# Kernel optimization log

Measured on AMD Instinct MI355X. Metric: run time of the kernel, lower is better.

## Reference

```python
import jax, jax.numpy as jnp
import numpy as np
from jax import lax

B, S, D = 8, 96, 768
R, RSEQ, TAG = 24, 8, 3


def setup_inputs() -> dict:
    key = jax.random.key(0)
    k0, k1, k2, k3 = jax.random.split(key, 4)
    encoded_text = jax.random.normal(k0, (B, S, D), jnp.float32)
    rel_types_encoded = jax.random.normal(k1, (R, RSEQ, D), jnp.float32)
    proj_W = jax.random.normal(k2, (2 * D, 3 * D), jnp.float32) * 0.02
    proj_b = jnp.zeros((3 * D,), jnp.float32)
    rel_W = jax.random.normal(k3, (3 * D, R * TAG), jnp.float32) * 0.02
    rel_b = jnp.zeros((R * TAG,), jnp.float32)
    return {
        "encoded_text": encoded_text,
        "rel_types_encoded": rel_types_encoded,
        "proj_W": proj_W,
        "proj_b": proj_b,
        "rel_W": rel_W,
        "rel_b": rel_b,
    }


def _refine(enc, rel_types):
    """Faithful vectorized version of the nested python loops in
    get_encoded_text: for each sample i, R sequential cross-attention
    updates on matrix_b using matrix_a = rel_types_encoded[i] (the
    original code indexes with i, reusing the same matrix_a each step).
    enc: [Bsz, S, D]; rel_types: [R, RSEQ, D].
    """
    Bsz = enc.shape[0]
    d = enc.shape[-1]
    scale = 1.0 / jnp.sqrt(jnp.asarray(d, enc.dtype))
    num_steps = rel_types.shape[0]  # loop runs rel_types_encoded.size(0) times
    A_batch = rel_types[:Bsz]  # matrix_a = rel_types_encoded[i]

    def per_sample(b0, A):  # b0: [S, D], A: [RSEQ, D]
        def step(b, _):
            scores = (A @ b.T) * scale            # [RSEQ, S]
            w = jax.nn.softmax(scores, axis=-1)    # softmax over seq
            return b + w.T @ A, None               # matrix_b += matrix_c
        bf, _ = lax.scan(step, b0, None, length=num_steps)
        return bf

    return jax.vmap(per_sample)(enc, A_batch)


def reference(encoded_text, rel_types_encoded, proj_W, proj_b, rel_W, rel_b):
    enc = _refine(encoded_text, rel_types_encoded)  # [B, S, D]
    Bsz, seq, d = enc.shape
    rel_num = rel_types_encoded.shape[0]
    tag_size = rel_W.shape[1] // rel_num

    # projection(cat(head, tail)) == head @ Wh + tail @ Wt + b; avoid
    # materializing the [B, S*S, 2D] concat (same math as the original).
    Wh, Wt = proj_W[:d], proj_W[d:]
    Hh = enc @ Wh                                   # [B, S, 3D] head part
    Ht = enc @ Wt                                   # [B, S, 3D] tail part
    pairs = Hh[:, :, None, :] + Ht[:, None, :, :] + proj_b  # [B, S, S, 3D]
    pairs = jax.nn.relu(pairs)
    triple = pairs.reshape(Bsz, seq * seq, 3 * d) @ rel_W + rel_b
    triple = triple.reshape(Bsz, seq, seq, rel_num, tag_size)
    return jnp.transpose(triple, (0, 4, 3, 1, 2))  # [B, tag, rel, S, S]
```

## Files before the change

kernel.cpp:

```cpp
#include <hip/hip_runtime.h>
#include <hip/hip_bf16.h>
#include <math.h>
#include <stdint.h>
#include <string.h>

#define BB 8
#define SS 96
#define DD 768
#define RR 24
#define RSEQ 8
#define TAG 3
#define D3 2304
#define NC 72

typedef __attribute__((ext_vector_type(8))) short bf16x8;
typedef __attribute__((ext_vector_type(4))) float f32x4;
typedef _Float16 f16x8 __attribute__((ext_vector_type(8)));
typedef _Float16 f16x2 __attribute__((ext_vector_type(2)));

typedef __attribute__((address_space(3))) uint8_t lds_u8;
typedef const __attribute__((address_space(1))) uint8_t glb_u8;
static __device__ __forceinline__ void glld16(const void* g, void* l) {
  __builtin_amdgcn_global_load_lds((glb_u8*)g, (lds_u8*)l, 16, 0, 0);
}

#define VMW(N) asm volatile("s_waitcnt vmcnt(" #N ")" ::: "memory")

static __device__ inline uint32_t pkrhu(float lo, float hi) {
  uint32_t a, b;
  memcpy(&a, &lo, 4);
  memcpy(&b, &hi, 4);
  return __builtin_amdgcn_perm(b + 0x8000u, a + 0x8000u, 0x07060302u);
}
static __device__ inline uint32_t pkrne(float lo, float hi) {
  uint32_t a, b;
  memcpy(&a, &lo, 4);
  memcpy(&b, &hi, 4);
  a += 0x7FFFu + ((a >> 16) & 1u);
  b += 0x7FFFu + ((b >> 16) & 1u);
  return (a >> 16) | (b & 0xFFFF0000u);
}
static __device__ inline uint32_t pkf16(float lo, float hi) {
  union { f16x2 h; uint32_t u; } r;
  r.h[0] = (_Float16)lo;
  r.h[1] = (_Float16)hi;
  return r.u;
}
static __device__ inline uint16_t f16b(float v) {
  union { _Float16 h; uint16_t u; } r;
  r.h = (_Float16)v;
  return r.u;
}

__global__ __launch_bounds__(256) void k_prep0(const float* __restrict__ relW,
                                               uint16_t* __restrict__ Wb,
                                               const float* __restrict__ projW,
                                               uint16_t* __restrict__ Tp,
                                               const float* __restrict__ enc,
                                               const float* __restrict__ rel,
                                               float* __restrict__ SG) {
  __shared__ __align__(16) char smem[24704];
  const int blk = blockIdx.x;
  const int t = threadIdx.x;

  if (blk < 36) {
    float* tile = (float*)smem;
    const int k0 = blk * 64;
    const float* src = relW + (size_t)k0 * NC;
    for (int e = t; e < 64 * NC / 4; e += 256) ((float4*)tile)[e] = ((const float4*)src)[e];
    __syncthreads();
    for (int u = t; u < 80 * 16; u += 256) {
      const int n = u >> 4, kq = (u & 15) * 4;
      uint2 w = {0u, 0u};
      if (n < NC) {
        w.x = pkf16(tile[(kq + 0) * NC + n], tile[(kq + 1) * NC + n]);
        w.y = pkf16(tile[(kq + 2) * NC + n], tile[(kq + 3) * NC + n]);
      }
      *(uint2*)&Wb[(size_t)n * D3 + k0 + kq] = w;
    }
  } else if (blk < 900) {
    const int bx = blk - 36;
    float (*tile)[65] = (float(*)[65])smem;
    const int c0 = (bx % 36) * 64;
    const int r0 = (bx / 36) * 64;
    {
      const int tr = t >> 4;
      const int tc4 = (t & 15) * 4;
#pragma unroll
      for (int p = 0; p < 4; ++p) {
        const int r = tr + p * 16;
        const float4 v = *(const float4*)&projW[(size_t)(r0 + r) * D3 + c0 + tc4];
        tile[r][tc4 + 0] = v.x;
        tile[r][tc4 + 1] = v.y;
        tile[r][tc4 + 2] = v.z;
        tile[r][tc4 + 3] = v.w;
      }
    }
    __syncthreads();
    {
      const int cc = t >> 4;
      const int rr4 = (t & 15) * 4;
#pragma unroll
      for (int p = 0; p < 4; ++p) {
        const int c = cc + p * 16;
        uint2 w;
        w.x = pkrne(tile[rr4 + 0][c], tile[rr4 + 1][c]);
        w.y = pkrne(tile[rr4 + 2][c], tile[rr4 + 3][c]);
        *(uint2*)&Tp[(size_t)(c0 + c) * (2 * DD) + r0 + rr4] = w;
      }
    }
  } else {
    const int idx = blk - 900;
    const int b = idx >> 4;
    const int d0 = (idx & 15) * 48;
    float (*AsF)[48] = (float(*)[48])smem;

    if (t < 96) {
      const int r = t / 12, q4 = (t % 12) * 4;
      *(float4*)&AsF[r][q4] = *(const float4*)&rel[((size_t)b * RSEQ + r) * DD + d0 + q4];
    }
    __syncthreads();

    for (int e = t; e < RSEQ * (SS + RSEQ); e += 256) {
      const int r = e & 7, s = e >> 3;
      const float* row = (s < SS) ? (enc + ((size_t)b * SS + s) * DD + d0) : &AsF[s - SS][0];
      float a0 = 0.f, a1 = 0.f, a2 = 0.f, a3 = 0.f;
#pragma unroll
      for (int d = 0; d < 48; d += 4) {
        const float4 rv = *(const float4*)&row[d];
        a0 += AsF[r][d + 0] * rv.x;
        a1 += AsF[r][d + 1] * rv.y;
        a2 += AsF[r][d + 2] * rv.z;
        a3 += AsF[r][d + 3] * rv.w;
      }
      atomicAdd(&SG[((size_t)b * RSEQ + r) * 104 + s], (a0 + a1) + (a2 + a3));
    }
  }
}

__global__ __launch_bounds__(256) void k_refS(const float* __restrict__ SG,
                                              float* __restrict__ Pst) {
  const int b = blockIdx.x;
  const int t = threadIdx.x;
  __shared__ float S0[RSEQ][SS];
  __shared__ float G[RSEQ][RSEQ];
  __shared__ float P[RSEQ][SS];
  __shared__ float sc[RSEQ][SS];
  const float scale = 0.036084391824351613f;

  for (int e = t; e < RSEQ * 104; e += 256) {
    const int r = e / 104, c = e % 104;
    const float v = SG[(size_t)b * RSEQ * 104 + e];
    if (c < SS) S0[r][c] = v;
    else G[r][c - SS] = v;
  }
  for (int e = t; e < RSEQ * SS; e += 256) ((float*)P)[e] = 0.f;
  __syncthreads();

  const int wave = t >> 6, lane = t & 63;
  for (int step = 0; step < RR; ++step) {
    for (int e = t; e < RSEQ * SS; e += 256) {
      const int r = e / SS, s = e % SS;
      float acc = S0[r][s];
#pragma unroll
      for (int r2 = 0; r2 < RSEQ; ++r2) acc += G[r][r2] * P[r2][s];
      sc[r][s] = acc * scale;
    }
    __syncthreads();
#pragma unroll
    for (int rr = 0; rr < 2; ++rr) {
      const int r = wave * 2 + rr;
      const float m1 = sc[r][lane];
      const float m2 = (lane < 32) ? sc[r][lane + 64] : -1e30f;
      float mx = fmaxf(m1, m2);
#pragma unroll
      for (int o = 32; o > 0; o >>= 1) mx = fmaxf(mx, __shfl_xor(mx, o, 64));
      const float e1 = __expf(m1 - mx);
      const float e2 = (lane < 32) ? __expf(m2 - mx) : 0.f;
      float sm = e1 + e2;
#pragma unroll
      for (int o = 32; o > 0; o >>= 1) sm += __shfl_xor(sm, o, 64);
      const float inv = 1.f / sm;
      P[r][lane] += e1 * inv;
      if (lane < 32) P[r][lane + 64] += e2 * inv;
    }
    __syncthreads();
  }

  for (int e = t; e < RSEQ * SS; e += 256) Pst[(size_t)b * RSEQ * SS + e] = ((float*)P)[e];
}

__global__ __launch_bounds__(256) void k_refB(const float* __restrict__ enc,
                                              const float* __restrict__ rel,
                                              const float* __restrict__ Pst,
                                              uint16_t* __restrict__ encRb) {
  const int blk = blockIdx.x;
  const int b = blk / 12;
  const int s0 = (blk % 12) * 8;
  const int t = threadIdx.x;
  __shared__ float As[RSEQ][DD + 4];
  __shared__ float Pl[RSEQ][8];

  const float* Ag = rel + (size_t)b * RSEQ * DD;
  for (int e = t; e < RSEQ * DD / 4; e += 256) {
    const int r = (e * 4) / DD, d = (e * 4) % DD;
    *(float4*)&As[r][d] = *(const float4*)&Ag[e * 4];
  }
  if (t < RSEQ * 8) {
    const int r = t >> 3, sl = t & 7;
    Pl[r][sl] = Pst[(size_t)b * RSEQ * SS + r * SS + s0 + sl];
  }
  __syncthreads();

  const float* Eb = enc + ((size_t)b * SS + s0) * DD;
  uint16_t* Ob = encRb + ((size_t)b * SS + s0) * DD;
  for (int e = t; e < 8 * DD / 4; e += 256) {
    const int sl = (e * 4) / DD, d = (e * 4) % DD;
    float4 v = ((const float4*)Eb)[e];
#pragma unroll
    for (int r = 0; r < RSEQ; ++r) {
      const float p = Pl[r][sl];
      v.x += p * As[r][d + 0];
      v.y += p * As[r][d + 1];
      v.z += p * As[r][d + 2];
      v.w += p * As[r][d + 3];
    }
    uint2 w;
    w.x = pkrhu(v.x, v.y);
    w.y = pkrhu(v.z, v.w);
    *(uint2*)&Ob[e * 4] = w;
  }
}

__global__ __launch_bounds__(256, 4) void k_proj(const uint16_t* __restrict__ Ab,
                                                 const uint16_t* __restrict__ Bt,
                                                 const float* __restrict__ pb,
                                                 uint16_t* __restrict__ Hh16,
                                                 uint16_t* __restrict__ Htf) {
  const int m0 = blockIdx.x * 64;
  const int gn0 = blockIdx.y * 64;
  const bool isH = gn0 < D3;
  const int n0 = isH ? gn0 : gn0 - D3;
  const int halfk = isH ? 0 : DD;
  const int t = threadIdx.x, w = t >> 6, lane = t & 63;
  const int wm = w >> 1, wn = w & 1;
  const int lm = lane & 15, q = lane >> 4;

  __shared__ __align__(16) uint16_t As[64 * 72];
  __shared__ __align__(16) uint16_t Bs[64 * 72];

  const char* rp[5];
  char* lp[5];
#pragma unroll
  for (int r = 0; r < 5; ++r) {
    const int idx = w + 4 * r;
    rp[r] = nullptr;
    lp[r] = nullptr;
    if (idx < 18) {
      const int ii = (idx < 9) ? idx : idx - 9;
      const int beta = ii * 1024 + lane * 16;
      const int elem = beta >> 1;
      const int row = elem / 72;
      int o = elem - row * 72;
      if (o >= 64) o = 0;
      if (idx < 9) {
        rp[r] = (const char*)(Ab + (size_t)(m0 + row) * DD + o);
        lp[r] = (char*)As + ii * 1024;
      } else {
        rp[r] = (const char*)(Bt + (size_t)(n0 + row) * (2 * DD) + halfk + o);
        lp[r] = (char*)Bs + ii * 1024;
      }
    }
  }

  f32x4 acc[2][2];
#pragma unroll
  for (int a = 0; a < 2; ++a)
#pragma unroll
    for (int c = 0; c < 2; ++c) acc[a][c] = (f32x4){0.f, 0.f, 0.f, 0.f};

  for (int k0 = 0; k0 < DD; k0 += 64) {
    __syncthreads();
#pragma unroll
    for (int r = 0; r < 5; ++r)
      if (rp[r]) glld16(rp[r] + 2 * k0, lp[r]);
    __syncthreads();
#pragma unroll
    for (int kk = 0; kk < 2; ++kk) {
      const int ko = kk * 32 + q * 8;
      bf16x8 af[2], bf[2];
#pragma unroll
      for (int mt = 0; mt < 2; ++mt)
        af[mt] = *(const bf16x8*)&As[(wm * 32 + mt * 16 + lm) * 72 + ko];
#pragma unroll
      for (int nt = 0; nt < 2; ++nt)
        bf[nt] = *(const bf16x8*)&Bs[(wn * 32 + nt * 16 + lm) * 72 + ko];
#pragma unroll
      for (int nt = 0; nt < 2; ++nt)
#pragma unroll
        for (int mt = 0; mt < 2; ++mt)
          acc[mt][nt] = __builtin_amdgcn_mfma_f32_16x16x32_bf16(af[mt], bf[nt], acc[mt][nt], 0, 0, 0);
    }
  }

#pragma unroll
  for (int nt = 0; nt < 2; ++nt) {
    const int ncol = n0 + wn * 32 + nt * 16 + lm;
    const int mrow = m0 + wm * 32 + q * 4;
    uint16_t* dst = isH ? Hh16 : Htf;
    const float bias = isH ? pb[ncol] : 0.f;
#pragma unroll
    for (int mt = 0; mt < 2; ++mt)
#pragma unroll
      for (int r = 0; r < 4; ++r)
        dst[(size_t)(mrow + mt * 16 + r) * D3 + ncol] = f16b(acc[mt][nt][r] + bias);
  }
}

#define HT_LDS 12288
#define BUF_B 22528
#define NISS 22
#define NKC 36

__global__ __launch_bounds__(384, 1) void k_pairs(const uint16_t* __restrict__ Hh,
                                                  const uint16_t* __restrict__ Htb,
                                                  const uint16_t* __restrict__ Wb,
                                                  const float* __restrict__ relb,
                                                  float* __restrict__ out) {
  const int blk = blockIdx.x;
  const int b = blk >> 5, ii = blk & 31;
  const int t = threadIdx.x;
  const int w = t >> 6, lane = t & 63;
  const int lm = lane & 15, q = lane >> 4;
  const int iw = w >> 1;
  const int jh = w & 1;
  const int i = ii * 3 + iw;

  __shared__ __align__(16) uint16_t Hr[7680];
  __shared__ __align__(16) uint16_t Stg[4][BUF_B / 2];

  {
    const char* hh = (const char*)(Hh + ((size_t)b * SS + ii * 3) * D3);
#pragma unroll
    for (int r = 0; r < 3; ++r) {
      const int idx = w + 6 * r;
      if (idx < 14) glld16(hh + idx * 1024 + lane * 16, (char*)Hr + idx * 1024);
    }
  }

  const char* rp[4];
#pragma unroll
  for (int r = 0; r < 4; ++r) {
    const int idx = w + 6 * r;
    rp[r] = nullptr;
    if (idx < NISS) {
      const int beta = idx * 1024 + lane * 16;
      if (beta < HT_LDS) {
        const int row = beta >> 7;
        const int real = (beta & 127) ^ ((row & 7) << 4);
        rp[r] = (const char*)(Htb + ((size_t)b * SS + row) * D3 + (real >> 1));
      } else {
        const int bb = beta - HT_LDS;
        const int row = bb >> 7;
        const int real = (bb & 127) ^ ((row & 7) << 4);
        rp[r] = (const char*)(Wb + (size_t)row * D3 + (real >> 1));
      }
    }
  }

#pragma unroll
  for (int c = 0; c < 2; ++c)
#pragma unroll
    for (int r = 0; r < 4; ++r)
      if (rp[r]) glld16(rp[r] + 128 * c, (char*)Stg[c] + (w + 6 * r) * 1024);

  f32x4 acc[3][5];
#pragma unroll
  for (int mt = 0; mt < 3; ++mt)
#pragma unroll
    for (int nt = 0; nt < 5; ++nt) acc[mt][nt] = (f32x4){0.f, 0.f, 0.f, 0.f};

  const f16x8 zro = {0, 0, 0, 0, 0, 0, 0, 0};

  for (int tc = 0; tc < NKC; ++tc) {
    {
      char* dst = (char*)Stg[(tc + 2) & 3];
      const int nc = (tc + 2 < NKC) ? (tc + 2) : (tc + 2 - NKC);
      const size_t koff = (size_t)128 * nc;
#pragma unroll
      for (int r = 0; r < 4; ++r)
        if (rp[r]) glld16(rp[r] + koff, dst + (w + 6 * r) * 1024);
    }
    if (w < 4) VMW(8); else VMW(6);
    __builtin_amdgcn_s_barrier();
    __builtin_amdgcn_sched_barrier(0);

    const char* S = (const char*)Stg[tc & 3];
    const int k0 = tc * 64;
#pragma unroll
    for (int kk = 0; kk < 2; ++kk) {
      const int ko = kk * 32 + q * 8;
      const int xb = (ko * 2) ^ ((lane & 7) << 4);
      const f16x8 hv = *(const f16x8*)&Hr[iw * D3 + k0 + ko];
      f16x8 af[3];
#pragma unroll
      for (int mt = 0; mt < 3; ++mt) {
        const f16x8 s = *(const f16x8*)(S + (jh * 48 + mt * 16 + lm) * 128 + xb) + hv;
        af[mt] = __builtin_elementwise_max(s, zro);
      }
      f16x8 bfv[5];
#pragma unroll
      for (int nt = 0; nt < 5; ++nt)
        bfv[nt] = *(const f16x8*)(S + HT_LDS + (nt * 16 + lm) * 128 + xb);
#pragma unroll
      for (int nt = 0; nt < 5; ++nt)
#pragma unroll
        for (int mt = 0; mt < 3; ++mt)
          acc[mt][nt] = __builtin_amdgcn_mfma_f32_16x16x32_f16(af[mt], bfv[nt], acc[mt][nt], 0, 0, 0);
    }
    asm volatile("s_waitcnt lgkmcnt(0)" ::: "memory");
    __builtin_amdgcn_sched_barrier(0);
  }

#pragma unroll
  for (int nt = 0; nt < 5; ++nt) {
    const int c = nt * 16 + lm;
    if (c < NC) {
      const float rb = relb[c];
      const int rr = c / 3, tg = c % 3;
#pragma unroll
      for (int mt = 0; mt < 3; ++mt) {
        const int j0 = jh * 48 + mt * 16 + q * 4;
        float* base = out + ((((size_t)b * TAG + tg) * RR + rr) * SS + i) * SS + j0;
        float4 o;
        o.x = acc[mt][nt][0] + rb;
        o.y = acc[mt][nt][1] + rb;
        o.z = acc[mt][nt][2] + rb;
        o.w = acc[mt][nt][3] + rb;
        *(float4*)base = o;
      }
    }
  }
}

extern "C" void kernel_launch(void* const* d_in, const int* in_sizes, int n_in,
                              void* d_out, int out_size, void* d_ws, size_t ws_size,
                              hipStream_t stream) {
  const float* enc   = (const float*)d_in[0];
  const float* rel   = (const float*)d_in[1];
  const float* projW = (const float*)d_in[2];
  const float* projb = (const float*)d_in[3];
  const float* relW  = (const float*)d_in[4];
  const float* relb  = (const float*)d_in[5];
  float* out = (float*)d_out;

  uint16_t* Hh16 = (uint16_t*)d_ws;
  uint16_t* Htf  = Hh16 + (size_t)DD * D3 + 512;
  uint16_t* Wb   = Htf + (size_t)DD * D3;
  uint16_t* Tp   = Wb + (size_t)96 * D3;
  uint16_t* Ab   = Tp + (size_t)D3 * 2 * DD;
  float* Pst = (float*)(Ab + (size_t)DD * DD);
  float* SG = Pst + (size_t)BB * RSEQ * SS;

  hipMemsetAsync(SG, 0, (size_t)BB * RSEQ * 104 * sizeof(float), stream);
  k_prep0<<<1028, 256, 0, stream>>>(relW, Wb, projW, Tp, enc, rel, SG);
  k_refS<<<BB, 256, 0, stream>>>(SG, Pst);
  k_refB<<<96, 256, 0, stream>>>(enc, rel, Pst, Ab);
  k_proj<<<dim3(12, 72), 256, 0, stream>>>(Ab, Tp, projb, Hh16, Htf);
  k_pairs<<<256, 384, 0, stream>>>(Hh16, Htf, Wb, relb, out);
}
```

Baseline: 187.2 us.

## Restage k_pairs pipeline into triple-buffered two-chunk phases with MFMA priority boost

New measurement: 186.5 us. About the same (-0.4%).

```diff
diff --git a/kernel.cpp b/kernel.cpp
--- a/kernel.cpp
+++ b/kernel.cpp
@@ -318,9 +318,10 @@
 }
 
 #define HT_LDS 12288
-#define BUF_B 22528
+#define CH_B 22528
 #define NISS 22
 #define NKC 36
+#define NPH 18
 
 __global__ __launch_bounds__(384, 1) void k_pairs(const uint16_t* __restrict__ Hh,
                                                   const uint16_t* __restrict__ Htb,
@@ -337,7 +338,7 @@
   const int i = ii * 3 + iw;
 
   __shared__ __align__(16) uint16_t Hr[7680];
-  __shared__ __align__(16) uint16_t Stg[4][BUF_B / 2];
+  __shared__ __align__(16) uint16_t Stg[3][CH_B];
 
   {
     const char* hh = (const char*)(Hh + ((size_t)b * SS + ii * 3) * D3);
@@ -369,10 +370,14 @@
   }
 
 #pragma unroll
-  for (int c = 0; c < 2; ++c)
-#pragma unroll
-    for (int r = 0; r < 4; ++r)
-      if (rp[r]) glld16(rp[r] + 128 * c, (char*)Stg[c] + (w + 6 * r) * 1024);
+  for (int pp = 0; pp < 2; ++pp)
+#pragma unroll
+    for (int kc = 0; kc < 2; ++kc)
+#pragma unroll
+      for (int r = 0; r < 4; ++r)
+        if (rp[r])
+          glld16(rp[r] + (size_t)128 * (2 * pp + kc),
+                 (char*)Stg[pp] + kc * CH_B + (w + 6 * r) * 1024);
 
   f32x4 acc[3][5];
 #pragma unroll
@@ -382,41 +387,52 @@
 
   const f16x8 zro = {0, 0, 0, 0, 0, 0, 0, 0};
 
-  for (int tc = 0; tc < NKC; ++tc) {
-    {
-      char* dst = (char*)Stg[(tc + 2) & 3];
-      const int nc = (tc + 2 < NKC) ? (tc + 2) : (tc + 2 - NKC);
-      const size_t koff = (size_t)128 * nc;
-#pragma unroll
-      for (int r = 0; r < 4; ++r)
-        if (rp[r]) glld16(rp[r] + koff, dst + (w + 6 * r) * 1024);
-    }
+  for (int p = 0; p < NPH; ++p) {
     if (w < 4) VMW(8); else VMW(6);
     __builtin_amdgcn_s_barrier();
     __builtin_amdgcn_sched_barrier(0);
 
-    const char* S = (const char*)Stg[tc & 3];
-    const int k0 = tc * 64;
-#pragma unroll
-    for (int kk = 0; kk < 2; ++kk) {
-      const int ko = kk * 32 + q * 8;
-      const int xb = (ko * 2) ^ ((lane & 7) << 4);
-      const f16x8 hv = *(const f16x8*)&Hr[iw * D3 + k0 + ko];
-      f16x8 af[3];
-#pragma unroll
-      for (int mt = 0; mt < 3; ++mt) {
-        const f16x8 s = *(const f16x8*)(S + (jh * 48 + mt * 16 + lm) * 128 + xb) + hv;
-        af[mt] = __builtin_elementwise_max(s, zro);
-      }
-      f16x8 bfv[5];
-#pragma unroll
-      for (int nt = 0; nt < 5; ++nt)
-        bfv[nt] = *(const f16x8*)(S + HT_LDS + (nt * 16 + lm) * 128 + xb);
-#pragma unroll
-      for (int nt = 0; nt < 5; ++nt)
-#pragma unroll
-        for (int mt = 0; mt < 3; ++mt)
-          acc[mt][nt] = __builtin_amdgcn_mfma_f32_16x16x32_f16(af[mt], bfv[nt], acc[mt][nt], 0, 0, 0);
+    {
+      char* dst = (char*)Stg[(p + 2) % 3];
+      int pn = p + 2;
+      if (pn >= NPH) pn -= NPH;
+#pragma unroll
+      for (int kc = 0; kc < 2; ++kc)
+#pragma unroll
+        for (int r = 0; r < 4; ++r)
+          if (rp[r])
+            glld16(rp[r] + (size_t)128 * (2 * pn + kc),
+                   dst + kc * CH_B + (w + 6 * r) * 1024);
+    }
+
+    const char* Sp = (const char*)Stg[p % 3];
+#pragma unroll
+    for (int kc = 0; kc < 2; ++kc) {
+      const char* S = Sp + kc * CH_B;
+      const int k0 = (2 * p + kc) * 64;
+#pragma unroll
+      for (int kk = 0; kk < 2; ++kk) {
+        const int ko = kk * 32 + q * 8;
+        const int xb = (ko * 2) ^ ((lane & 7) << 4);
+        const f16x8 hv = *(const f16x8*)&Hr[iw * D3 + k0 + ko];
+        f16x8 af[3];
+#pragma unroll
+        for (int mt = 0; mt < 3; ++mt) {
+          const f16x8 s = *(const f16x8*)(S + (jh * 48 + mt * 16 + lm) * 128 + xb) + hv;
+          af[mt] = __builtin_elementwise_max(s, zro);
+        }
+        f16x8 bfv[5];
+#pragma unroll
+        for (int nt = 0; nt < 5; ++nt)
+          bfv[nt] = *(const f16x8*)(S + HT_LDS + (nt * 16 + lm) * 128 + xb);
+        __builtin_amdgcn_s_setprio(1);
+#pragma unroll
+        for (int nt = 0; nt < 5; ++nt)
+#pragma unroll
+          for (int mt = 0; mt < 3; ++mt)
+            acc[mt][nt] = __builtin_amdgcn_mfma_f32_16x16x32_f16(af[mt], bfv[nt], acc[mt][nt], 0, 0, 0);
+        __builtin_amdgcn_s_setprio(0);
+      }
     }
     asm volatile("s_waitcnt lgkmcnt(0)" ::: "memory");
     __builtin_amdgcn_sched_barrier(0);
```
